# Kernel optimization log

Hardware: AMD Instinct MI355X
Metric: run time of the kernel (lower is better)

## Reference

```python
import jax, jax.numpy as jnp
import numpy as np

B, IH, IW = 16, 32, 32
N = IH * IW
HEADS, DIM_HEAD = 8, 64
INNER = HEADS * DIM_HEAD  # 512
INP, OUP = 512, 512
SCALE = DIM_HEAD ** -0.5


def _relative_index():
    # replicate torch.meshgrid (ij) -> coords [2, N]
    yy, xx = np.meshgrid(np.arange(IH), np.arange(IW), indexing='ij')
    coords = np.stack([yy.reshape(-1), xx.reshape(-1)])  # [2, N]
    rel = coords[:, :, None] - coords[:, None, :]        # [2, N, N]
    rel[0] += IH - 1
    rel[1] += IW - 1
    rel[0] *= 2 * IW - 1
    return jnp.asarray(rel.sum(0).reshape(-1), dtype=jnp.int32)  # [N*N]


def setup_inputs() -> dict:
    key = jax.random.key(0)
    k1, k2, k3, k4, k5 = jax.random.split(key, 5)
    x = jax.random.normal(k1, (B, N, INP), dtype=jnp.float32)
    W_qkv = jax.random.normal(k2, (INP, 3 * INNER), dtype=jnp.float32) * (INP ** -0.5)
    # table is initialized to zeros in the module; use small randn so bias path is exercised
    rel_table = jax.random.normal(k3, ((2 * IH - 1) * (2 * IW - 1), HEADS), dtype=jnp.float32) * 0.02
    W_out = jax.random.normal(k4, (INNER, OUP), dtype=jnp.float32) * (INNER ** -0.5)
    b_out = jax.random.normal(k5, (OUP,), dtype=jnp.float32) * 0.02
    return {
        'x': x,
        'W_qkv': W_qkv,
        'rel_table': rel_table,
        'W_out': W_out,
        'b_out': b_out,
        'rel_index': _relative_index(),
    }


def reference(x, W_qkv, rel_table, W_out, b_out, rel_index):
    b, n, _ = x.shape
    qkv = x @ W_qkv                                            # [b, n, 3*inner]
    q, k, v = jnp.split(qkv, 3, axis=-1)
    def to_heads(t):
        return t.reshape(b, n, HEADS, DIM_HEAD).transpose(0, 2, 1, 3)  # [b, h, n, d]
    q, k, v = to_heads(q), to_heads(k), to_heads(v)
    dots = jnp.einsum('bhnd,bhmd->bhnm', q, k) * SCALE         # [b, h, n, n]
    bias = rel_table[rel_index].reshape(n, n, HEADS).transpose(2, 0, 1)[None]  # [1, h, n, n]
    attn = jax.nn.softmax(dots + bias, axis=-1)
    out = jnp.einsum('bhnm,bhmd->bhnd', attn, v)               # [b, h, n, d]
    out = out.transpose(0, 2, 1, 3).reshape(b, n, INNER)       # [b, n, inner]
    return out @ W_out + b_out
```

## Files before the change

kernel.cpp:

```cpp
#include <hip/hip_runtime.h>
#include <math.h>

#define BATCH 16
#define NTOK 1024
#define HEADS 8
#define DHEAD 64
#define INNER 512
#define QKV_COLS 1536
#define SCALE_L2E 0.1803368801111244f
#define LOG2E 1.4426950408889634f

#if __has_builtin(__builtin_amdgcn_exp2f)
#define EXP2F(x) __builtin_amdgcn_exp2f(x)
#else
#define EXP2F(x) __expf((x) * 0.6931471805599453f)
#endif

typedef _Float16 f16x8 __attribute__((ext_vector_type(8)));
typedef _Float16 f16x4 __attribute__((ext_vector_type(4)));
typedef float f32x4 __attribute__((ext_vector_type(4)));

#define MFMA32(a, b, c) __builtin_amdgcn_mfma_f32_16x16x32_f16(a, b, c, 0, 0, 0)

__device__ __forceinline__ void glds16(const void* g, void* l) {
    __builtin_amdgcn_global_load_lds(
        (const __attribute__((address_space(1))) unsigned int*)g,
        (__attribute__((address_space(3))) unsigned int*)l, 16, 0, 0);
}

#define XV (BATCH * NTOK * INNER / 4)
#define XB (XV / 256)
#define WQTILES 192
#define WOTILES 64

__global__ __launch_bounds__(256)
void convert_inputs(const float* __restrict__ x, const float* __restrict__ Wq,
                    const float* __restrict__ Wo, _Float16* __restrict__ x_h,
                    _Float16* __restrict__ Wq_t, _Float16* __restrict__ Wo_t) {
    const int b = blockIdx.x, t = threadIdx.x;
    if (b < XB) {
        const int idx = b * 256 + t;
        float4 v = ((const float4*)x)[idx];
        f16x4 h;
        h[0] = (_Float16)v.x; h[1] = (_Float16)v.y;
        h[2] = (_Float16)v.z; h[3] = (_Float16)v.w;
        *(f16x4*)(x_h + (size_t)idx * 4) = h;
        return;
    }
    const bool isQ = (b < XB + WQTILES);
    const int b2  = isQ ? (b - XB) : (b - XB - WQTILES);
    const int ntl = isQ ? 24 : 8;
    const int ldw = isQ ? QKV_COLS : INNER;
    const float*   W  = isQ ? Wq   : Wo;
    _Float16*      Wt = isQ ? Wq_t : Wo_t;
    const int k0 = (b2 / ntl) * 64, n0 = (b2 % ntl) * 64;
    const int kk = k0 + (t >> 4) * 4, nn = n0 + (t & 15) * 4;
    f32x4 v0 = *(const f32x4*)(W + (size_t)(kk + 0) * ldw + nn);
    f32x4 v1 = *(const f32x4*)(W + (size_t)(kk + 1) * ldw + nn);
    f32x4 v2 = *(const f32x4*)(W + (size_t)(kk + 2) * ldw + nn);
    f32x4 v3 = *(const f32x4*)(W + (size_t)(kk + 3) * ldw + nn);
#pragma unroll
    for (int f = 0; f < 4; ++f) {
        f16x4 h;
        h[0] = (_Float16)v0[f]; h[1] = (_Float16)v1[f];
        h[2] = (_Float16)v2[f]; h[3] = (_Float16)v3[f];
        *(f16x4*)(Wt + (size_t)(nn + f) * INNER + kk) = h;
    }
}

__global__ __launch_bounds__(256, 3)
void gemm_qkv(const _Float16* __restrict__ A, const _Float16* __restrict__ Bt,
              _Float16* __restrict__ qkv, _Float16* __restrict__ vtg,
              int M, int N, int K) {
    __shared__ _Float16 As[3][128 * 32];
    __shared__ _Float16 Bs[3][128 * 32];

    const int t    = threadIdx.x;
    const int l    = t & 63;
    const int w    = t >> 6;
    const int wm   = w >> 1;
    const int wn   = w & 1;
    const int quad = l >> 4;
    const int lrow = l & 15;

    const int nwg = gridDim.x * gridDim.y;
    int bid = blockIdx.x + gridDim.x * blockIdx.y;
    bid = (bid & 7) * (nwg >> 3) + (bid >> 3);
    const size_t row0 = (size_t)(bid / gridDim.x) * 128;
    const size_t col0 = (size_t)(bid % gridDim.x) * 128;

    const int srow = t >> 2;
    const int sch  = t & 3;

    f32x4 acc[4][4] = {};
    const int NSTEP = K >> 5;

    auto stage = [&](int kk, int bufi) {
#pragma unroll
        for (int p = 0; p < 2; ++p) {
            const int r  = p * 64 + srow;
            const int gc = (sch ^ ((r >> 1) & 3)) * 8;
            glds16(A  + (row0 + r) * K + kk * 32 + gc, (char*)As[bufi] + p * 4096 + t * 16);
            glds16(Bt + (col0 + r) * K + kk * 32 + gc, (char*)Bs[bufi] + p * 4096 + t * 16);
        }
    };

    stage(0, 0);
    stage(1, 1);

    int buf = 0, pre = 2;
    for (int kk = 0; kk < NSTEP; ++kk) {
        if (kk + 1 < NSTEP) asm volatile("s_waitcnt vmcnt(4)" ::: "memory");
        else                asm volatile("s_waitcnt vmcnt(0)" ::: "memory");
        __builtin_amdgcn_s_barrier();
        __builtin_amdgcn_sched_barrier(0);
        if (kk + 2 < NSTEP) stage(kk + 2, pre);

        f16x8 af[4], bf[4];
#pragma unroll
        for (int i = 0; i < 4; ++i) {
            const int r = wm * 64 + i * 16 + lrow;
            af[i] = *(const f16x8*)(As[buf] + r * 32 + ((quad ^ ((r >> 1) & 3)) * 8));
        }
#pragma unroll
        for (int j = 0; j < 4; ++j) {
            const int r = wn * 64 + j * 16 + lrow;
            bf[j] = *(const f16x8*)(Bs[buf] + r * 32 + ((quad ^ ((r >> 1) & 3)) * 8));
        }
#pragma unroll
        for (int i = 0; i < 4; ++i)
#pragma unroll
            for (int j = 0; j < 4; ++j)
                acc[i][j] = MFMA32(bf[j], af[i], acc[i][j]);

        buf = (buf == 2) ? 0 : buf + 1;
        pre = (pre == 2) ? 0 : pre + 1;
    }

    const bool isV = (col0 >= 2 * INNER);
#pragma unroll
    for (int i = 0; i < 4; ++i) {
        const size_t m = row0 + wm * 64 + i * 16 + lrow;
#pragma unroll
        for (int j = 0; j < 4; ++j) {
            const size_t c = col0 + wn * 64 + j * 16 + quad * 4;
            f32x4 v = acc[i][j];
            if (!isV) {
                f16x4 hv;
                hv[0] = (_Float16)v[0]; hv[1] = (_Float16)v[1];
                hv[2] = (_Float16)v[2]; hv[3] = (_Float16)v[3];
                *(f16x4*)(qkv + m * N + c) = hv;
            } else {
                const int cv = (int)(c - 2 * INNER);
                const int hh = cv >> 6, db = cv & 63;
                const size_t vb = (((size_t)(m >> 10) * HEADS + hh) * 64 + db) * NTOK
                                  + (m & (NTOK - 1));
#pragma unroll
                for (int reg = 0; reg < 4; ++reg)
                    vtg[vb + (size_t)reg * NTOK] = (_Float16)v[reg];
            }
        }
    }
}

__global__ __launch_bounds__(256, 3)
void gemm_out(const _Float16* __restrict__ A, const _Float16* __restrict__ Bt,
              const float* __restrict__ bias, float* __restrict__ Cout,
              int M, int N, int K) {
    __shared__ _Float16 As[3][128 * 32];
    __shared__ _Float16 Bs[3][128 * 32];

    const int t    = threadIdx.x;
    const int l    = t & 63;
    const int w    = t >> 6;
    const int wm   = w >> 1;
    const int wn   = w & 1;
    const int quad = l >> 4;
    const int lrow = l & 15;

    const int nwg = gridDim.x * gridDim.y;
    int bid = blockIdx.x + gridDim.x * blockIdx.y;
    bid = (bid & 7) * (nwg >> 3) + (bid >> 3);
    const size_t row0 = (size_t)(bid / gridDim.x) * 128;
    const size_t col0 = (size_t)(bid % gridDim.x) * 128;

    const int srow = t >> 2;
    const int sch  = t & 3;

    f32x4 acc[4][4] = {};
    const int NSTEP = K >> 5;

    auto stage = [&](int kk, int bufi) {
#pragma unroll
        for (int p = 0; p < 2; ++p) {
            const int r  = p * 64 + srow;
            const int gc = (sch ^ ((r >> 1) & 3)) * 8;
            glds16(A  + (row0 + r) * K + kk * 32 + gc, (char*)As[bufi] + p * 4096 + t * 16);
            glds16(Bt + (col0 + r) * K + kk * 32 + gc, (char*)Bs[bufi] + p * 4096 + t * 16);
        }
    };

    stage(0, 0);
    stage(1, 1);

    int buf = 0, pre = 2;
    for (int kk = 0; kk < NSTEP; ++kk) {
        if (kk + 1 < NSTEP) asm volatile("s_waitcnt vmcnt(4)" ::: "memory");
        else                asm volatile("s_waitcnt vmcnt(0)" ::: "memory");
        __builtin_amdgcn_s_barrier();
        __builtin_amdgcn_sched_barrier(0);
        if (kk + 2 < NSTEP) stage(kk + 2, pre);

        f16x8 af[4], bf[4];
#pragma unroll
        for (int i = 0; i < 4; ++i) {
            const int r = wm * 64 + i * 16 + lrow;
            af[i] = *(const f16x8*)(As[buf] + r * 32 + ((quad ^ ((r >> 1) & 3)) * 8));
        }
#pragma unroll
        for (int j = 0; j < 4; ++j) {
            const int r = wn * 64 + j * 16 + lrow;
            bf[j] = *(const f16x8*)(Bs[buf] + r * 32 + ((quad ^ ((r >> 1) & 3)) * 8));
        }
#pragma unroll
        for (int i = 0; i < 4; ++i)
#pragma unroll
            for (int j = 0; j < 4; ++j)
                acc[i][j] = MFMA32(bf[j], af[i], acc[i][j]);

        buf = (buf == 2) ? 0 : buf + 1;
        pre = (pre == 2) ? 0 : pre + 1;
    }

#pragma unroll
    for (int i = 0; i < 4; ++i) {
        const size_t m = row0 + wm * 64 + i * 16 + lrow;
#pragma unroll
        for (int j = 0; j < 4; ++j) {
            const size_t c = col0 + wn * 64 + j * 16 + quad * 4;
            f32x4 v = acc[i][j];
            float4 bv = *(const float4*)(bias + c);
            v[0] += bv.x; v[1] += bv.y; v[2] += bv.z; v[3] += bv.w;
            *(f32x4*)(Cout + m * N + c) = v;
        }
    }
}

__global__ __launch_bounds__(512, 4)
void attn_f16_v7(const _Float16* __restrict__ qkv, const _Float16* __restrict__ vt,
                 const float* __restrict__ rel_table, _Float16* __restrict__ out) {
    __shared__ _Float16 Ks[2][64 * 64];
    __shared__ _Float16 Vs[2][64 * 64];
    __shared__ float biasS[3969];

    const int t    = threadIdx.x;
    const int l    = t & 63;
    const int w    = t >> 6;
    const int quad = l >> 4;
    const int lrow = l & 15;
    const int h    = blockIdx.y;
    const int bb   = blockIdx.z;
    const int qr0  = blockIdx.x * 256 + w * 32;

    for (int idx = t; idx < 3969; idx += 512)
        biasS[idx] = rel_table[idx * HEADS + h] * LOG2E;

    const size_t tokbase = (size_t)bb * NTOK;

    f16x8 aq[2][2];
#pragma unroll
    for (int mt = 0; mt < 2; ++mt)
#pragma unroll
        for (int ksi = 0; ksi < 2; ++ksi)
            aq[mt][ksi] = *(const f16x8*)(qkv + (tokbase + qr0 + mt * 16 + lrow) * QKV_COLS
                                          + h * DHEAD + ksi * 32 + quad * 8);

    f32x4 O[2][4] = {};
    float l0 = 0.f, l1 = 0.f;

    const int iy = qr0 >> 5;
    const int krow_base = 8 * (lrow >> 2) + (lrow & 3);
    const int fKl = (lrow & 3) + 4 * ((lrow >> 2) & 1);

    const int kr  = t >> 3;
    const int ksl = t & 7;
    const int fKr = (kr & 3) + 4 * ((kr >> 3) & 1);
    const _Float16* kbase = qkv + tokbase * QKV_COLS + INNER + h * DHEAD;
    const _Float16* vbase = vt + ((size_t)(bb * HEADS + h) * 64) * NTOK;

    auto stage = [&](int jt, int bufi) {
        const int j0s = jt * 64;
        glds16(kbase + (size_t)(j0s + kr) * QKV_COLS + (ksl ^ fKr) * 8, (char*)Ks[bufi] + t * 16);
        glds16(vbase + (size_t)kr * NTOK + j0s + (ksl ^ (kr & 7)) * 8,  (char*)Vs[bufi] + t * 16);
    };

    stage(0, 0);

    for (int jt = 0; jt < 16; ++jt) {
        const int buf = jt & 1;
        __syncthreads();
        if (jt < 15) stage(jt + 1, buf ^ 1);

#pragma unroll
        for (int jn0 = 0; jn0 < 2; ++jn0) {
            f16x8 pb0, pb1;
#pragma unroll
            for (int s = 0; s < 2; ++s) {
                const int krow = jn0 * 32 + krow_base + 4 * s;
                f32x4 S0 = {}, S1 = {};
                __builtin_amdgcn_s_setprio(1);
#pragma unroll
                for (int ksi = 0; ksi < 2; ++ksi) {
                    f16x8 bk = *(const f16x8*)(Ks[buf] + krow * 64
                                               + (((ksi * 4 + quad) ^ fKl) * 8));
                    S0 = MFMA32(bk, aq[0][ksi], S0);
                    S1 = MFMA32(bk, aq[1][ksi], S1);
                }
                __builtin_amdgcn_s_setprio(0);
                const int base = (iy - (jt * 2 + jn0) + 31) * 63 + 31 + lrow
                                 - 8 * quad - 4 * s;
                {
                    float p0 = EXP2F(fmaf(S0[0], SCALE_L2E, biasS[base - 0]));
                    float p1 = EXP2F(fmaf(S0[1], SCALE_L2E, biasS[base - 1]));
                    float p2 = EXP2F(fmaf(S0[2], SCALE_L2E, biasS[base - 2]));
                    float p3 = EXP2F(fmaf(S0[3], SCALE_L2E, biasS[base - 3]));
                    l0 += (p0 + p1) + (p2 + p3);
                    pb0[s * 4 + 0] = (_Float16)p0; pb0[s * 4 + 1] = (_Float16)p1;
                    pb0[s * 4 + 2] = (_Float16)p2; pb0[s * 4 + 3] = (_Float16)p3;
                }
                {
                    const int b1 = base + 16;
                    float p0 = EXP2F(fmaf(S1[0], SCALE_L2E, biasS[b1 - 0]));
                    float p1 = EXP2F(fmaf(S1[1], SCALE_L2E, biasS[b1 - 1]));
                    float p2 = EXP2F(fmaf(S1[2], SCALE_L2E, biasS[b1 - 2]));
                    float p3 = EXP2F(fmaf(S1[3], SCALE_L2E, biasS[b1 - 3]));
                    l1 += (p0 + p1) + (p2 + p3);
                    pb1[s * 4 + 0] = (_Float16)p0; pb1[s * 4 + 1] = (_Float16)p1;
                    pb1[s * 4 + 2] = (_Float16)p2; pb1[s * 4 + 3] = (_Float16)p3;
                }
            }

            __builtin_amdgcn_s_setprio(1);
#pragma unroll
            for (int dn = 0; dn < 4; ++dn) {
                const int d = dn * 16 + lrow;
                f16x8 av = *(const f16x8*)(Vs[buf] + d * 64
                              + (((jn0 * 4 + quad) ^ (d & 7)) * 8));
                O[0][dn] = MFMA32(av, pb0, O[0][dn]);
                O[1][dn] = MFMA32(av, pb1, O[1][dn]);
            }
            __builtin_amdgcn_s_setprio(0);
        }
    }

#pragma unroll
    for (int mt = 0; mt < 2; ++mt) {
        float s = mt ? l1 : l0;
        s += __shfl_xor(s, 16);
        s += __shfl_xor(s, 32);
        const float inv = 1.f / s;
        const size_t orow = (tokbase + qr0 + mt * 16 + lrow) * INNER + h * DHEAD;
#pragma unroll
        for (int dn = 0; dn < 4; ++dn) {
            const f32x4 o = O[mt][dn];
            f16x4 ov;
            ov[0] = (_Float16)(o[0] * inv); ov[1] = (_Float16)(o[1] * inv);
            ov[2] = (_Float16)(o[2] * inv); ov[3] = (_Float16)(o[3] * inv);
            *(f16x4*)(out + orow + dn * 16 + quad * 4) = ov;
        }
    }
}

extern "C" void kernel_launch(void* const* d_in, const int* in_sizes, int n_in,
                              void* d_out, int out_size, void* d_ws, size_t ws_size,
                              hipStream_t stream) {
    const float* x         = (const float*)d_in[0];
    const float* W_qkv     = (const float*)d_in[1];
    const float* rel_table = (const float*)d_in[2];
    const float* W_out     = (const float*)d_in[3];
    const float* b_out     = (const float*)d_in[4];

    _Float16* x_h   = (_Float16*)d_ws;
    _Float16* Wq_t  = x_h + (size_t)BATCH * NTOK * INNER;
    _Float16* Wo_t  = Wq_t + (size_t)INNER * QKV_COLS;
    _Float16* qkv_h = Wo_t + (size_t)INNER * INNER;
    _Float16* att_h = qkv_h + (size_t)BATCH * NTOK * QKV_COLS;
    _Float16* vt_g  = att_h + (size_t)BATCH * NTOK * INNER;

    const int M = BATCH * NTOK;

    convert_inputs<<<XB + WQTILES + WOTILES, 256, 0, stream>>>(
        x, W_qkv, W_out, x_h, Wq_t, Wo_t);

    gemm_qkv<<<dim3(QKV_COLS / 128, M / 128), 256, 0, stream>>>(
        x_h, Wq_t, qkv_h, vt_g, M, QKV_COLS, INNER);

    attn_f16_v7<<<dim3(NTOK / 256, HEADS, BATCH), 512, 0, stream>>>(
        qkv_h, vt_g, rel_table, att_h);

    gemm_out<<<dim3(INNER / 128, M / 128), 256, 0, stream>>>(
        att_h, Wo_t, b_out, (float*)d_out, M, INNER, INNER);
}
```

Measured before the change: 208.9 us.

## Fuse fp32-to-fp16 conversion of x into the QKV GEMM loads

Removes the separate pass that converts x to fp16; the QKV GEMM now streams fp32 x tiles into LDS and converts them to fp16 in registers before the MFMAs. This avoids writing and re-reading an fp16 copy of x. In exchange each GEMM tile loads twice the bytes for A, the LDS pipeline drops from three stages to two with a plain __syncthreads, and extra conversion instructions are added in the inner loop.

After: 207.4 us. About the same (-0.7%).

```diff
diff --git a/kernel.cpp b/kernel.cpp
--- a/kernel.cpp
+++ b/kernel.cpp
@@ -28,27 +28,15 @@
         (__attribute__((address_space(3))) unsigned int*)l, 16, 0, 0);
 }
 
-#define XV (BATCH * NTOK * INNER / 4)
-#define XB (XV / 256)
 #define WQTILES 192
 #define WOTILES 64
 
 __global__ __launch_bounds__(256)
-void convert_inputs(const float* __restrict__ x, const float* __restrict__ Wq,
-                    const float* __restrict__ Wo, _Float16* __restrict__ x_h,
-                    _Float16* __restrict__ Wq_t, _Float16* __restrict__ Wo_t) {
+void convert_w(const float* __restrict__ Wq, const float* __restrict__ Wo,
+               _Float16* __restrict__ Wq_t, _Float16* __restrict__ Wo_t) {
     const int b = blockIdx.x, t = threadIdx.x;
-    if (b < XB) {
-        const int idx = b * 256 + t;
-        float4 v = ((const float4*)x)[idx];
-        f16x4 h;
-        h[0] = (_Float16)v.x; h[1] = (_Float16)v.y;
-        h[2] = (_Float16)v.z; h[3] = (_Float16)v.w;
-        *(f16x4*)(x_h + (size_t)idx * 4) = h;
-        return;
-    }
-    const bool isQ = (b < XB + WQTILES);
-    const int b2  = isQ ? (b - XB) : (b - XB - WQTILES);
+    const bool isQ = (b < WQTILES);
+    const int b2  = isQ ? b : (b - WQTILES);
     const int ntl = isQ ? 24 : 8;
     const int ldw = isQ ? QKV_COLS : INNER;
     const float*   W  = isQ ? Wq   : Wo;
@@ -69,11 +57,11 @@
 }
 
 __global__ __launch_bounds__(256, 3)
-void gemm_qkv(const _Float16* __restrict__ A, const _Float16* __restrict__ Bt,
+void gemm_qkv(const float* __restrict__ Af, const _Float16* __restrict__ Bt,
               _Float16* __restrict__ qkv, _Float16* __restrict__ vtg,
               int M, int N, int K) {
-    __shared__ _Float16 As[3][128 * 32];
-    __shared__ _Float16 Bs[3][128 * 32];
+    __shared__ float    Asf[2][128 * 32];
+    __shared__ _Float16 Bs[2][128 * 32];
 
     const int t    = threadIdx.x;
     const int l    = t & 63;
@@ -89,38 +77,49 @@
     const size_t row0 = (size_t)(bid / gridDim.x) * 128;
     const size_t col0 = (size_t)(bid % gridDim.x) * 128;
 
-    const int srow = t >> 2;
-    const int sch  = t & 3;
+    const int arow = t >> 3;
+    const int ach  = t & 7;
+    const int brow = t >> 2;
+    const int bch  = t & 3;
 
     f32x4 acc[4][4] = {};
     const int NSTEP = K >> 5;
 
     auto stage = [&](int kk, int bufi) {
 #pragma unroll
+        for (int p = 0; p < 4; ++p) {
+            const int r  = p * 32 + arow;
+            const int gc = (ach ^ (r & 7)) * 4;
+            glds16(Af + (row0 + r) * K + kk * 32 + gc,
+                   (char*)Asf[bufi] + p * 4096 + t * 16);
+        }
+#pragma unroll
         for (int p = 0; p < 2; ++p) {
-            const int r  = p * 64 + srow;
-            const int gc = (sch ^ ((r >> 1) & 3)) * 8;
-            glds16(A  + (row0 + r) * K + kk * 32 + gc, (char*)As[bufi] + p * 4096 + t * 16);
-            glds16(Bt + (col0 + r) * K + kk * 32 + gc, (char*)Bs[bufi] + p * 4096 + t * 16);
+            const int r  = p * 64 + brow;
+            const int gc = (bch ^ ((r >> 1) & 3)) * 8;
+            glds16(Bt + (col0 + r) * K + kk * 32 + gc,
+                   (char*)Bs[bufi] + p * 4096 + t * 16);
         }
     };
 
     stage(0, 0);
-    stage(1, 1);
-
-    int buf = 0, pre = 2;
+
     for (int kk = 0; kk < NSTEP; ++kk) {
-        if (kk + 1 < NSTEP) asm volatile("s_waitcnt vmcnt(4)" ::: "memory");
-        else                asm volatile("s_waitcnt vmcnt(0)" ::: "memory");
-        __builtin_amdgcn_s_barrier();
-        __builtin_amdgcn_sched_barrier(0);
-        if (kk + 2 < NSTEP) stage(kk + 2, pre);
+        const int buf = kk & 1;
+        __syncthreads();
+        if (kk + 1 < NSTEP) stage(kk + 1, buf ^ 1);
 
         f16x8 af[4], bf[4];
 #pragma unroll
         for (int i = 0; i < 4; ++i) {
             const int r = wm * 64 + i * 16 + lrow;
-            af[i] = *(const f16x8*)(As[buf] + r * 32 + ((quad ^ ((r >> 1) & 3)) * 8));
+            f32x4 a0 = *(const f32x4*)(Asf[buf] + r * 32 + (((2 * quad) ^ (r & 7)) * 4));
+            f32x4 a1 = *(const f32x4*)(Asf[buf] + r * 32 + (((2 * quad + 1) ^ (r & 7)) * 4));
+#pragma unroll
+            for (int e = 0; e < 4; ++e) {
+                af[i][e]     = (_Float16)a0[e];
+                af[i][4 + e] = (_Float16)a1[e];
+            }
         }
 #pragma unroll
         for (int j = 0; j < 4; ++j) {
@@ -132,9 +131,6 @@
 #pragma unroll
             for (int j = 0; j < 4; ++j)
                 acc[i][j] = MFMA32(bf[j], af[i], acc[i][j]);
-
-        buf = (buf == 2) ? 0 : buf + 1;
-        pre = (pre == 2) ? 0 : pre + 1;
     }
 
     const bool isV = (col0 >= 2 * INNER);
@@ -380,8 +376,7 @@
     const float* W_out     = (const float*)d_in[3];
     const float* b_out     = (const float*)d_in[4];
 
-    _Float16* x_h   = (_Float16*)d_ws;
-    _Float16* Wq_t  = x_h + (size_t)BATCH * NTOK * INNER;
+    _Float16* Wq_t  = (_Float16*)d_ws;
     _Float16* Wo_t  = Wq_t + (size_t)INNER * QKV_COLS;
     _Float16* qkv_h = Wo_t + (size_t)INNER * INNER;
     _Float16* att_h = qkv_h + (size_t)BATCH * NTOK * QKV_COLS;
@@ -389,11 +384,10 @@
 
     const int M = BATCH * NTOK;
 
-    convert_inputs<<<XB + WQTILES + WOTILES, 256, 0, stream>>>(
-        x, W_qkv, W_out, x_h, Wq_t, Wo_t);
+    convert_w<<<WQTILES + WOTILES, 256, 0, stream>>>(W_qkv, W_out, Wq_t, Wo_t);
 
     gemm_qkv<<<dim3(QKV_COLS / 128, M / 128), 256, 0, stream>>>(
-        x_h, Wq_t, qkv_h, vt_g, M, QKV_COLS, INNER);
+        x, Wq_t, qkv_h, vt_g, M, QKV_COLS, INNER);
 
     attn_f16_v7<<<dim3(NTOK / 256, HEADS, BATCH), 512, 0, stream>>>(
         qkv_h, vt_g, rel_table, att_h);
```
